# Kernel optimization log

Measured on AMD Instinct MI355X. Metric: run time of the kernel, lower is better.

The kernel has to match this reference:

```python
import jax, jax.numpy as jnp
import numpy as np

N_DST = 50000


def setup_inputs() -> dict:
    key = jax.random.key(0)
    k1, k2, k3, k4, k5, k6 = jax.random.split(key, 6)
    n_src, n_dst, n_edges, d_in, d_out = 50000, 50000, 1600000, 128, 128
    return {
        "h_neigh": jax.random.normal(k1, (n_src, d_in), dtype=jnp.float32),
        "h_self": jax.random.normal(k2, (n_dst, d_in), dtype=jnp.float32),
        "src_idx": jax.random.randint(k3, (n_edges,), 0, n_src, dtype=jnp.int32),
        "dst_idx": jax.random.randint(k4, (n_edges,), 0, n_dst, dtype=jnp.int32),
        "W_self": jax.random.normal(k5, (d_out, d_in), dtype=jnp.float32) * 0.05,
        "W_neigh": jax.random.normal(k6, (d_out, d_in), dtype=jnp.float32) * 0.05,
    }


def reference(h_neigh, h_self, src_idx, dst_idx, W_self, W_neigh):
    # mean aggregation over edges: for each dst node, mean of src features
    msgs = h_neigh[src_idx]                                   # [E, d_in]
    summed = jax.ops.segment_sum(msgs, dst_idx, num_segments=N_DST)  # [N_dst, d_in]
    deg = jax.ops.segment_sum(jnp.ones_like(dst_idx, dtype=h_neigh.dtype),
                              dst_idx, num_segments=N_DST)    # [N_dst]
    agg = summed / jnp.maximum(deg, 1.0)[:, None]             # mean; 0 for isolated nodes

    z = h_self @ W_self.T + agg @ W_neigh.T                   # [N_dst, d_out]
    z = jax.nn.relu(z)
    # L2 normalize rows, guarding zero norms
    z_norm = jnp.linalg.norm(z, axis=1, keepdims=True)
    z_norm = jnp.where(z_norm == 0, 1.0, z_norm)
    return z / z_norm
```

## Files before the change

### kernel.cpp

```cpp
#include <hip/hip_runtime.h>
#include <hip/hip_bf16.h>

#define DFEAT 128
#define BSH 7
#define CAP 4608

typedef short short8 __attribute__((ext_vector_type(8)));
typedef float f32x4 __attribute__((ext_vector_type(4)));

__global__ void convert_bf16_kernel(const float2* __restrict__ in,
                                    __hip_bfloat162* __restrict__ out, int n2) {
    int i = blockIdx.x * blockDim.x + threadIdx.x;
    if (i < n2) {
        float2 v = in[i];
        __hip_bfloat162 o;
        o.x = __float2bfloat16(v.x);
        o.y = __float2bfloat16(v.y);
        out[i] = o;
    }
}

__global__ void wcat_init_kernel(const float* __restrict__ Wself, const float* __restrict__ Wneigh,
                                 unsigned short* __restrict__ wcat, int* __restrict__ gcursor) {
    int idx = blockIdx.x * 256 + threadIdx.x;
    int j = idx >> 8, k = idx & 255;
    float v = (k < DFEAT) ? Wself[j * DFEAT + k] : Wneigh[j * DFEAT + k - DFEAT];
    __hip_bfloat16 h = __float2bfloat16(v);
    wcat[idx] = *(unsigned short*)&h;
    if (blockIdx.x < 2) {
        int b = blockIdx.x * 256 + threadIdx.x;
        gcursor[b] = b * CAP;
    }
}

__global__ void partition_kernel(const int* __restrict__ src, const int* __restrict__ dst,
                                 int E, int* __restrict__ gcursor,
                                 unsigned* __restrict__ pairs) {
    __shared__ int hist[512];
    __shared__ int base[512];
    int tid = threadIdx.x;
    for (int b0 = blockIdx.x * 2048; b0 < E; b0 += gridDim.x * 2048) {
        hist[tid] = 0;
        hist[tid + 256] = 0;
        __syncthreads();
        unsigned mypk[8];
        int mybin[8], myrank[8];
#pragma unroll
        for (int e = 0; e < 8; ++e) {
            int i = b0 + e * 256 + tid;
            mybin[e] = -1;
            if (i < E) {
                unsigned d = (unsigned)dst[i];
                unsigned s = (unsigned)src[i];
                int bin = d >> BSH;
                mybin[e] = bin;
                myrank[e] = atomicAdd(&hist[bin], 1);
                mypk[e] = (d << 16) | s;
            }
        }
        __syncthreads();
        if (hist[tid]) base[tid] = atomicAdd(&gcursor[tid], hist[tid]);
        if (hist[tid + 256]) base[tid + 256] = atomicAdd(&gcursor[tid + 256], hist[tid + 256]);
        __syncthreads();
#pragma unroll
        for (int e = 0; e < 8; ++e)
            if (mybin[e] >= 0) pairs[base[mybin[e]] + myrank[e]] = mypk[e];
        __syncthreads();
    }
}

__global__ void fine_fill_kernel(const unsigned* __restrict__ pairs,
                                 const int* __restrict__ gcursor,
                                 int* __restrict__ row_start, int* __restrict__ deg,
                                 unsigned short* __restrict__ csr16, int n_dst) {
    __shared__ int hist[256];
    __shared__ int cur[256];
    __shared__ int wtot[4];
    int b = blockIdx.x;
    int tid = threadIdx.x;
    int lo = b * CAP, hi = gcursor[b];
    hist[tid] = 0;
    __syncthreads();
    for (int j = lo + tid; j < hi; j += 256)
        atomicAdd(&hist[(pairs[j] >> 16) & 127], 1);
    __syncthreads();
    int v = hist[tid];
    int lane = tid & 63, w = tid >> 6;
    int x = v;
    for (int off = 1; off < 64; off <<= 1) {
        int t = __shfl_up(x, off);
        if (lane >= off) x += t;
    }
    if (lane == 63) wtot[w] = x;
    __syncthreads();
    if (tid == 0) {
        int r = 0;
        for (int i = 0; i < 4; ++i) { int t = wtot[i]; wtot[i] = r; r += t; }
    }
    __syncthreads();
    int excl = x + wtot[w] - v;
    cur[tid] = excl;
    int d = (b << BSH) + tid;
    if (tid < (1 << BSH) && d < n_dst) {
        row_start[d] = lo + excl;
        deg[d] = v;
    }
    __syncthreads();
    for (int j = lo + tid; j < hi; j += 256) {
        unsigned p = pairs[j];
        int slot = atomicAdd(&cur[(p >> 16) & 127], 1);
        csr16[lo + slot] = (unsigned short)(p & 0xFFFFu);
    }
}

template <int PASS>
__global__ void aggregate_kernel(const unsigned short* __restrict__ hnb,
                                 const unsigned short* __restrict__ csr16,
                                 const int* __restrict__ row_start,
                                 const int* __restrict__ deg,
                                 unsigned short* __restrict__ agb, int n_dst) {
    int gtid = blockIdx.x * blockDim.x + threadIdx.x;
    int d = gtid >> 6;
    int lane = gtid & 63;
    if (d >= n_dst) return;
    int beg = row_start[d];
    int dg = deg[d];
    int slot = lane >> 4;
    int fg = lane & 15;
    float a0 = 0.f, a1 = 0.f, a2 = 0.f, a3 = 0.f;
    for (int base = 0; base < dg; base += 64) {
        int cnt = dg - base;
        if (cnt > 64) cnt = 64;
        int s = (base + lane < dg) ? (int)csr16[beg + base + lane] : 0;
        for (int j = 0; j < cnt; j += 8) {
            int e0 = j + slot;
            int e1 = e0 + 4;
            int i0 = __shfl(s, e0);
            int i1 = __shfl(s, e1 & 63);
            const ushort4* p0 = (const ushort4*)(hnb + i0 * DFEAT + PASS * 64 + fg * 4);
            const ushort4* p1 = (const ushort4*)(hnb + i1 * DFEAT + PASS * 64 + fg * 4);
            ushort4 v0 = *p0;
            ushort4 v1 = *p1;
            if (e0 < cnt) {
                a0 += __bfloat162float(*(__hip_bfloat16*)&v0.x);
                a1 += __bfloat162float(*(__hip_bfloat16*)&v0.y);
                a2 += __bfloat162float(*(__hip_bfloat16*)&v0.z);
                a3 += __bfloat162float(*(__hip_bfloat16*)&v0.w);
            }
            if (e1 < cnt) {
                a0 += __bfloat162float(*(__hip_bfloat16*)&v1.x);
                a1 += __bfloat162float(*(__hip_bfloat16*)&v1.y);
                a2 += __bfloat162float(*(__hip_bfloat16*)&v1.z);
                a3 += __bfloat162float(*(__hip_bfloat16*)&v1.w);
            }
        }
    }
    a0 += __shfl_xor(a0, 16); a0 += __shfl_xor(a0, 32);
    a1 += __shfl_xor(a1, 16); a1 += __shfl_xor(a1, 32);
    a2 += __shfl_xor(a2, 16); a2 += __shfl_xor(a2, 32);
    a3 += __shfl_xor(a3, 16); a3 += __shfl_xor(a3, 32);
    if (lane < 16) {
        float inv = 1.0f / (float)(dg > 1 ? dg : 1);
        __hip_bfloat16 b0 = __float2bfloat16(a0 * inv);
        __hip_bfloat16 b1 = __float2bfloat16(a1 * inv);
        __hip_bfloat16 b2 = __float2bfloat16(a2 * inv);
        __hip_bfloat16 b3 = __float2bfloat16(a3 * inv);
        ushort4 o;
        o.x = *(unsigned short*)&b0;
        o.y = *(unsigned short*)&b1;
        o.z = *(unsigned short*)&b2;
        o.w = *(unsigned short*)&b3;
        *(ushort4*)(agb + d * DFEAT + PASS * 64 + lane * 4) = o;
    }
}

__launch_bounds__(512, 4)
__global__ void gemm_mfma_kernel(const float* __restrict__ h_self,
                                 const unsigned short* __restrict__ agb,
                                 const unsigned short* __restrict__ Wcat,
                                 float* __restrict__ out, int M) {
    __shared__ char Ws[64 * 1024];
    int tid = threadIdx.x;
    int row0 = blockIdx.x * 128;
    {
        int j = tid >> 2, q = tid & 3;
#pragma unroll
        for (int u = 0; u < 8; ++u) {
            int ks = q * 64 + u * 8;
            uint4 vv = *(const uint4*)(Wcat + j * 256 + ks);
            *(uint4*)(Ws + ((j * 512 + ks * 2) ^ ((j & 7) << 4))) = vv;
        }
    }
    __syncthreads();

    int lane = tid & 63, w = tid >> 6;
    int arow = row0 + w * 16 + (lane & 15);
    int kgrp = (lane >> 4) * 8;
    bool rv = arow < M;
    int ar = rv ? arow : 0;

    f32x4 acc[8] = {};
#pragma unroll
    for (int kstep = 0; kstep < 8; ++kstep) {
        int kk = kstep * 32 + kgrp;
        short8 a;
        if (kk < DFEAT) {
            float4 f0 = *(const float4*)(h_self + (size_t)ar * DFEAT + kk);
            float4 f1 = *(const float4*)(h_self + (size_t)ar * DFEAT + kk + 4);
            __hip_bfloat16 b0 = __float2bfloat16(f0.x), b1 = __float2bfloat16(f0.y);
            __hip_bfloat16 b2 = __float2bfloat16(f0.z), b3 = __float2bfloat16(f0.w);
            __hip_bfloat16 b4 = __float2bfloat16(f1.x), b5 = __float2bfloat16(f1.y);
            __hip_bfloat16 b6 = __float2bfloat16(f1.z), b7 = __float2bfloat16(f1.w);
            a[0] = *(short*)&b0; a[1] = *(short*)&b1; a[2] = *(short*)&b2; a[3] = *(short*)&b3;
            a[4] = *(short*)&b4; a[5] = *(short*)&b5; a[6] = *(short*)&b6; a[7] = *(short*)&b7;
        } else {
            a = *(const short8*)(agb + (size_t)ar * DFEAT + (kk - DFEAT));
        }
#pragma unroll
        for (int n = 0; n < 8; ++n) {
            int nr = n * 16 + (lane & 15);
            short8 bfrag = *(const short8*)(Ws + ((nr * 512 + kk * 2) ^ ((nr & 7) << 4)));
            acc[n] = __builtin_amdgcn_mfma_f32_16x16x32_bf16(a, bfrag, acc[n], 0, 0, 0);
        }
    }

    float ss[4] = {0.f, 0.f, 0.f, 0.f};
#pragma unroll
    for (int n = 0; n < 8; ++n)
#pragma unroll
        for (int i = 0; i < 4; ++i) {
            float z = fmaxf(acc[n][i], 0.f);
            acc[n][i] = z;
            ss[i] += z * z;
        }
#pragma unroll
    for (int i = 0; i < 4; ++i)
        for (int m = 1; m < 16; m <<= 1) ss[i] += __shfl_xor(ss[i], m);
#pragma unroll
    for (int i = 0; i < 4; ++i) {
        int grow = row0 + w * 16 + (lane >> 4) * 4 + i;
        if (grow < M) {
            float nv = sqrtf(ss[i]);
            float inv = (nv == 0.f) ? 1.f : 1.f / nv;
#pragma unroll
            for (int n = 0; n < 8; ++n)
                out[(size_t)grow * DFEAT + n * 16 + (lane & 15)] = acc[n][i] * inv;
        }
    }
}

extern "C" void kernel_launch(void* const* d_in, const int* in_sizes, int n_in,
                              void* d_out, int out_size, void* d_ws, size_t ws_size,
                              hipStream_t stream) {
    const float* h_neigh = (const float*)d_in[0];
    const float* h_self  = (const float*)d_in[1];
    const int*   src_idx = (const int*)d_in[2];
    const int*   dst_idx = (const int*)d_in[3];
    const float* W_self  = (const float*)d_in[4];
    const float* W_neigh = (const float*)d_in[5];
    float* out = (float*)d_out;

    const int D = DFEAT;
    int n_src = in_sizes[0] / D;
    int n_dst = in_sizes[1] / D;
    int E = in_sizes[2];
    int NB = (n_dst + (1 << BSH) - 1) >> BSH;

    char* wsp = (char*)d_ws;
    size_t off = 0;
    auto alloc = [&](size_t bytes) -> void* {
        void* p = wsp + off;
        off += (bytes + 255) & ~(size_t)255;
        return p;
    };
    int* gcursor          = (int*)alloc(512 * 4);
    int* row_start        = (int*)alloc((size_t)n_dst * 4);
    int* deg              = (int*)alloc((size_t)n_dst * 4);
    unsigned* pairs       = (unsigned*)alloc((size_t)NB * CAP * 4);
    unsigned short* csr16 = (unsigned short*)alloc((size_t)NB * CAP * 2 + 256);
    unsigned short* hnb   = (unsigned short*)alloc((size_t)n_src * D * 2);
    unsigned short* agb   = (unsigned short*)alloc((size_t)n_dst * D * 2);
    unsigned short* wcat  = (unsigned short*)alloc((size_t)DFEAT * 256 * 2);
    (void)ws_size;

    convert_bf16_kernel<<<(n_src * (D / 2) + 255) / 256, 256, 0, stream>>>(
        (const float2*)h_neigh, (__hip_bfloat162*)hnb, n_src * (D / 2));

    wcat_init_kernel<<<128, 256, 0, stream>>>(W_self, W_neigh, wcat, gcursor);

    partition_kernel<<<256, 256, 0, stream>>>(src_idx, dst_idx, E, gcursor, pairs);

    fine_fill_kernel<<<NB, 256, 0, stream>>>(pairs, gcursor, row_start, deg, csr16, n_dst);

    int agg_blocks = (n_dst * 64 + 255) / 256;
    aggregate_kernel<0><<<agg_blocks, 256, 0, stream>>>(hnb, csr16, row_start, deg, agb, n_dst);
    aggregate_kernel<1><<<agg_blocks, 256, 0, stream>>>(hnb, csr16, row_start, deg, agb, n_dst);

    gemm_mfma_kernel<<<(n_dst + 127) / 128, 512, 0, stream>>>(
        h_self, agb, wcat, out, n_dst);
}
```

Baseline: 128.8 us.

## Merge prep kernels, single-shot partition, and 4-way feature-split aggregation in one launch

Fuses the bf16 conversion and weight-concat/cursor init into one prep launch. Partition now handles 4096 edges per block in a single pass, with one block per chunk instead of a grid-stride loop. Aggregation is split into four 32-feature slices through blockIdx.y in one launch, with 8 edges in flight per iteration instead of 4. The aim is to cut launch overhead and shrink each slice's gathered working set so it stays cache-resident, at the cost of more redundant index loads and an extra shuffle-reduction stage.

Result: slower. 142.8 us (+10.8%).

```diff
diff --git a/kernel.cpp b/kernel.cpp
--- a/kernel.cpp
+++ b/kernel.cpp
@@ -8,28 +8,32 @@
 typedef short short8 __attribute__((ext_vector_type(8)));
 typedef float f32x4 __attribute__((ext_vector_type(4)));
 
-__global__ void convert_bf16_kernel(const float2* __restrict__ in,
-                                    __hip_bfloat162* __restrict__ out, int n2) {
-    int i = blockIdx.x * blockDim.x + threadIdx.x;
-    if (i < n2) {
-        float2 v = in[i];
-        __hip_bfloat162 o;
-        o.x = __float2bfloat16(v.x);
-        o.y = __float2bfloat16(v.y);
-        out[i] = o;
-    }
-}
-
-__global__ void wcat_init_kernel(const float* __restrict__ Wself, const float* __restrict__ Wneigh,
-                                 unsigned short* __restrict__ wcat, int* __restrict__ gcursor) {
-    int idx = blockIdx.x * 256 + threadIdx.x;
-    int j = idx >> 8, k = idx & 255;
-    float v = (k < DFEAT) ? Wself[j * DFEAT + k] : Wneigh[j * DFEAT + k - DFEAT];
-    __hip_bfloat16 h = __float2bfloat16(v);
-    wcat[idx] = *(unsigned short*)&h;
-    if (blockIdx.x < 2) {
-        int b = blockIdx.x * 256 + threadIdx.x;
-        gcursor[b] = b * CAP;
+__global__ void prep_kernel(const float2* __restrict__ in, __hip_bfloat162* __restrict__ out,
+                            int n2, int nconv,
+                            const float* __restrict__ Wself, const float* __restrict__ Wneigh,
+                            unsigned short* __restrict__ wcat, int* __restrict__ gcursor) {
+    int b = blockIdx.x;
+    int tid = threadIdx.x;
+    if (b < nconv) {
+        int i = b * 256 + tid;
+        if (i < n2) {
+            float2 v = in[i];
+            __hip_bfloat162 o;
+            o.x = __float2bfloat16(v.x);
+            o.y = __float2bfloat16(v.y);
+            out[i] = o;
+        }
+    } else {
+        int bb = b - nconv;
+        int idx = bb * 256 + tid;
+        int j = idx >> 8, k = idx & 255;
+        float v = (k < DFEAT) ? Wself[j * DFEAT + k] : Wneigh[j * DFEAT + k - DFEAT];
+        __hip_bfloat16 h = __float2bfloat16(v);
+        wcat[idx] = *(unsigned short*)&h;
+        if (bb < 2) {
+            int s = bb * 256 + tid;
+            gcursor[s] = s * CAP;
+        }
     }
 }
 
@@ -39,34 +43,32 @@
     __shared__ int hist[512];
     __shared__ int base[512];
     int tid = threadIdx.x;
-    for (int b0 = blockIdx.x * 2048; b0 < E; b0 += gridDim.x * 2048) {
-        hist[tid] = 0;
-        hist[tid + 256] = 0;
-        __syncthreads();
-        unsigned mypk[8];
-        int mybin[8], myrank[8];
-#pragma unroll
-        for (int e = 0; e < 8; ++e) {
-            int i = b0 + e * 256 + tid;
-            mybin[e] = -1;
-            if (i < E) {
-                unsigned d = (unsigned)dst[i];
-                unsigned s = (unsigned)src[i];
-                int bin = d >> BSH;
-                mybin[e] = bin;
-                myrank[e] = atomicAdd(&hist[bin], 1);
-                mypk[e] = (d << 16) | s;
-            }
-        }
-        __syncthreads();
-        if (hist[tid]) base[tid] = atomicAdd(&gcursor[tid], hist[tid]);
-        if (hist[tid + 256]) base[tid + 256] = atomicAdd(&gcursor[tid + 256], hist[tid + 256]);
-        __syncthreads();
-#pragma unroll
-        for (int e = 0; e < 8; ++e)
-            if (mybin[e] >= 0) pairs[base[mybin[e]] + myrank[e]] = mypk[e];
-        __syncthreads();
-    }
+    int b0 = blockIdx.x * 4096;
+    hist[tid] = 0;
+    hist[tid + 256] = 0;
+    __syncthreads();
+    unsigned mypk[16];
+    int mybin[16], myrank[16];
+#pragma unroll
+    for (int e = 0; e < 16; ++e) {
+        int i = b0 + e * 256 + tid;
+        mybin[e] = -1;
+        if (i < E) {
+            unsigned d = (unsigned)dst[i];
+            unsigned s = (unsigned)src[i];
+            int bin = d >> BSH;
+            mybin[e] = bin;
+            myrank[e] = atomicAdd(&hist[bin], 1);
+            mypk[e] = (d << 16) | s;
+        }
+    }
+    __syncthreads();
+    if (hist[tid]) base[tid] = atomicAdd(&gcursor[tid], hist[tid]);
+    if (hist[tid + 256]) base[tid + 256] = atomicAdd(&gcursor[tid + 256], hist[tid + 256]);
+    __syncthreads();
+#pragma unroll
+    for (int e = 0; e < 16; ++e)
+        if (mybin[e] >= 0) pairs[base[mybin[e]] + myrank[e]] = mypk[e];
 }
 
 __global__ void fine_fill_kernel(const unsigned* __restrict__ pairs,
@@ -113,7 +115,6 @@
     }
 }
 
-template <int PASS>
 __global__ void aggregate_kernel(const unsigned short* __restrict__ hnb,
                                  const unsigned short* __restrict__ csr16,
                                  const int* __restrict__ row_start,
@@ -121,26 +122,26 @@
                                  unsigned short* __restrict__ agb, int n_dst) {
     int gtid = blockIdx.x * blockDim.x + threadIdx.x;
     int d = gtid >> 6;
-    int lane = gtid & 63;
     if (d >= n_dst) return;
+    int lane = threadIdx.x & 63;
+    int pass = blockIdx.y;
     int beg = row_start[d];
     int dg = deg[d];
-    int slot = lane >> 4;
-    int fg = lane & 15;
+    int slot = lane >> 3;
+    int fl = lane & 7;
+    const unsigned short* tab = hnb + pass * 32 + fl * 4;
     float a0 = 0.f, a1 = 0.f, a2 = 0.f, a3 = 0.f;
     for (int base = 0; base < dg; base += 64) {
         int cnt = dg - base;
         if (cnt > 64) cnt = 64;
         int s = (base + lane < dg) ? (int)csr16[beg + base + lane] : 0;
-        for (int j = 0; j < cnt; j += 8) {
+        for (int j = 0; j < cnt; j += 16) {
             int e0 = j + slot;
-            int e1 = e0 + 4;
-            int i0 = __shfl(s, e0);
+            int e1 = j + 8 + slot;
+            int i0 = __shfl(s, e0 & 63);
             int i1 = __shfl(s, e1 & 63);
-            const ushort4* p0 = (const ushort4*)(hnb + i0 * DFEAT + PASS * 64 + fg * 4);
-            const ushort4* p1 = (const ushort4*)(hnb + i1 * DFEAT + PASS * 64 + fg * 4);
-            ushort4 v0 = *p0;
-            ushort4 v1 = *p1;
+            ushort4 v0 = *(const ushort4*)(tab + i0 * DFEAT);
+            ushort4 v1 = *(const ushort4*)(tab + i1 * DFEAT);
             if (e0 < cnt) {
                 a0 += __bfloat162float(*(__hip_bfloat16*)&v0.x);
                 a1 += __bfloat162float(*(__hip_bfloat16*)&v0.y);
@@ -155,11 +156,11 @@
             }
         }
     }
-    a0 += __shfl_xor(a0, 16); a0 += __shfl_xor(a0, 32);
-    a1 += __shfl_xor(a1, 16); a1 += __shfl_xor(a1, 32);
-    a2 += __shfl_xor(a2, 16); a2 += __shfl_xor(a2, 32);
-    a3 += __shfl_xor(a3, 16); a3 += __shfl_xor(a3, 32);
-    if (lane < 16) {
+    a0 += __shfl_xor(a0, 8); a0 += __shfl_xor(a0, 16); a0 += __shfl_xor(a0, 32);
+    a1 += __shfl_xor(a1, 8); a1 += __shfl_xor(a1, 16); a1 += __shfl_xor(a1, 32);
+    a2 += __shfl_xor(a2, 8); a2 += __shfl_xor(a2, 16); a2 += __shfl_xor(a2, 32);
+    a3 += __shfl_xor(a3, 8); a3 += __shfl_xor(a3, 16); a3 += __shfl_xor(a3, 32);
+    if (lane < 8) {
         float inv = 1.0f / (float)(dg > 1 ? dg : 1);
         __hip_bfloat16 b0 = __float2bfloat16(a0 * inv);
         __hip_bfloat16 b1 = __float2bfloat16(a1 * inv);
@@ -170,7 +171,7 @@
         o.y = *(unsigned short*)&b1;
         o.z = *(unsigned short*)&b2;
         o.w = *(unsigned short*)&b3;
-        *(ushort4*)(agb + d * DFEAT + PASS * 64 + lane * 4) = o;
+        *(ushort4*)(agb + d * DFEAT + pass * 32 + lane * 4) = o;
     }
 }
 
@@ -283,18 +284,19 @@
     unsigned short* wcat  = (unsigned short*)alloc((size_t)DFEAT * 256 * 2);
     (void)ws_size;
 
-    convert_bf16_kernel<<<(n_src * (D / 2) + 255) / 256, 256, 0, stream>>>(
-        (const float2*)h_neigh, (__hip_bfloat162*)hnb, n_src * (D / 2));
-
-    wcat_init_kernel<<<128, 256, 0, stream>>>(W_self, W_neigh, wcat, gcursor);
-
-    partition_kernel<<<256, 256, 0, stream>>>(src_idx, dst_idx, E, gcursor, pairs);
+    int n2 = n_src * (D / 2);
+    int nconv = (n2 + 255) / 256;
+    prep_kernel<<<nconv + 128, 256, 0, stream>>>(
+        (const float2*)h_neigh, (__hip_bfloat162*)hnb, n2, nconv,
+        W_self, W_neigh, wcat, gcursor);
+
+    partition_kernel<<<(E + 4095) / 4096, 256, 0, stream>>>(
+        src_idx, dst_idx, E, gcursor, pairs);
 
     fine_fill_kernel<<<NB, 256, 0, stream>>>(pairs, gcursor, row_start, deg, csr16, n_dst);
 
-    int agg_blocks = (n_dst * 64 + 255) / 256;
-    aggregate_kernel<0><<<agg_blocks, 256, 0, stream>>>(hnb, csr16, row_start, deg, agb, n_dst);
-    aggregate_kernel<1><<<agg_blocks, 256, 0, stream>>>(hnb, csr16, row_start, deg, agb, n_dst);
+    dim3 agrid((n_dst * 64 + 255) / 256, 4);
+    aggregate_kernel<<<agrid, 256, 0, stream>>>(hnb, csr16, row_start, deg, agb, n_dst);
 
     gemm_mfma_kernel<<<(n_dst + 127) / 128, 512, 0, stream>>>(
         h_self, agb, wcat, out, n_dst);
```
